# Kernel tuning notes

Hardware: AMD Instinct MI355X
Metric: run time of the kernel (lower is better)

The kernel has to match this reference:

```python
import jax, jax.numpy as jnp
import numpy as np

# Config (matches init_kwargs + Mamba2 defaults: expand=2, headdim=64, ngroups=1)
B_, C_IN, T, H, W = 4, 23, 8, 128, 128
P = 4
DM = 256
D_STATE = 16
D_CONV = 4
EXPAND = 2
D_INNER = EXPAND * DM            # 512
HEADDIM = 64
NHEADS = D_INNER // HEADDIM      # 8
CONV_DIM = D_INNER + 2 * D_STATE # 544 (ngroups=1)
D_IN_PROJ = 2 * D_INNER + 2 * D_STATE + NHEADS


def setup_inputs() -> dict:
    key = jax.random.key(0)
    ks = jax.random.split(key, 12)
    s = lambda k, shape, sc: (jax.random.normal(k, shape, jnp.float32) * sc)
    x = jax.random.normal(ks[0], (B_, C_IN, T, H, W), jnp.float32)
    patch_w = s(ks[1], (DM, C_IN, P, P), 0.05)       # Conv3d weight, depth-1 dim squeezed
    patch_b = s(ks[2], (DM,), 0.02)
    W_in = s(ks[3], (DM, D_IN_PROJ), 0.05)           # in_proj (bias=False)
    conv_w = s(ks[4], (CONV_DIM, D_CONV), 0.2)       # depthwise conv1d weight
    conv_b = s(ks[5], (CONV_DIM,), 0.02)
    dt_bias = jnp.log(jnp.expm1(jnp.exp(jax.random.uniform(ks[6], (NHEADS,), jnp.float32, jnp.log(1e-3), jnp.log(1e-1)))))
    A_log = jnp.log(jnp.arange(1, NHEADS + 1, dtype=jnp.float32))
    D_param = jnp.ones((NHEADS,), jnp.float32)
    norm_w = jnp.ones((D_INNER,), jnp.float32)
    W_out = s(ks[7], (D_INNER, DM), 0.05)            # out_proj (bias=False)
    unembed_w = s(ks[8], (DM, C_IN, P, P), 0.05)     # ConvTranspose3d weight (in,out,1,p,p)
    unembed_b = s(ks[9], (C_IN,), 0.02)
    return {"x": x, "patch_w": patch_w, "patch_b": patch_b, "W_in": W_in,
            "conv_w": conv_w, "conv_b": conv_b, "dt_bias": dt_bias, "A_log": A_log,
            "D_param": D_param, "norm_w": norm_w, "W_out": W_out,
            "unembed_w": unembed_w, "unembed_b": unembed_b}


def reference(x, patch_w, patch_b, W_in, conv_w, conv_b, dt_bias, A_log,
              D_param, norm_w, W_out, unembed_w, unembed_b):
    B, C, Tt, Hh, Ww = x.shape
    p = patch_w.shape[-1]
    Hp, Wp = Hh // p, Ww // p
    L = Tt * Hp * Wp
    # --- Conv3d patch embed (kernel (1,p,p), stride (1,p,p)) == non-overlapping patchify ---
    xr = x.reshape(B, C, Tt, Hp, p, Wp, p)
    emb = jnp.einsum('bcthiwj,dcij->bthwd', xr, patch_w) + patch_b  # [B,T,Hp,Wp,D]
    xs = emb.reshape(B, L, DM)
    # --- Mamba2 ---
    zxbcdt = xs @ W_in                                 # [B,L,2*d_inner+2*d_state+nheads]
    z = zxbcdt[:, :, :D_INNER]
    xBC = zxbcdt[:, :, D_INNER:D_INNER + CONV_DIM]
    dt = zxbcdt[:, :, D_INNER + CONV_DIM:]             # [B,L,nheads]
    # causal depthwise conv1d + silu
    xp = jnp.pad(xBC, ((0, 0), (D_CONV - 1, 0), (0, 0)))
    conv_out = conv_b + sum(xp[:, k:k + L, :] * conv_w[:, k] for k in range(D_CONV))
    xBC = jax.nn.silu(conv_out)
    xh = xBC[:, :, :D_INNER].reshape(B, L, NHEADS, HEADDIM)
    Bm = xBC[:, :, D_INNER:D_INNER + D_STATE]          # [B,L,N] (ngroups=1)
    Cm = xBC[:, :, D_INNER + D_STATE:]                 # [B,L,N]
    dt = jax.nn.softplus(dt + dt_bias)                 # [B,L,H]
    A = -jnp.exp(A_log)                                # [H]
    dA = jnp.exp(dt * A)                               # [B,L,H]
    xdt = xh * dt[..., None]                           # [B,L,H,P]
    # selective state-space scan: h_t = dA_t h_{t-1} + (dt_t x_t) B_t^T ; y_t = h_t C_t
    def step(h, inp):
        dA_t, xdt_t, B_t, C_t = inp
        h = dA_t[..., None, None] * h + jnp.einsum('bhp,bn->bhpn', xdt_t, B_t)
        y = jnp.einsum('bhpn,bn->bhp', h, C_t)
        return h, y
    inps = (dA.transpose(1, 0, 2), xdt.transpose(1, 0, 2, 3),
            Bm.transpose(1, 0, 2), Cm.transpose(1, 0, 2))
    h0 = jnp.zeros((B, NHEADS, HEADDIM, D_STATE), xs.dtype)
    _, ys = jax.lax.scan(step, h0, inps)               # [L,B,H,P]
    y = ys.transpose(1, 0, 2, 3) + D_param[None, None, :, None] * xh
    y = y.reshape(B, L, D_INNER)
    # gated RMSNorm (norm_before_gate=False): rmsnorm(y * silu(z)) * w
    yg = y * jax.nn.silu(z)
    y = yg * jax.lax.rsqrt(jnp.mean(yg * yg, axis=-1, keepdims=True) + 1e-5) * norm_w
    out_seq = y @ W_out                                # [B,L,DM]
    # --- ConvTranspose3d unembed (kernel (1,p,p), stride (1,p,p)) == un-patchify ---
    outp = out_seq.reshape(B, Tt, Hp, Wp, DM)
    un = jnp.einsum('bthwd,dcij->bcthiwj', outp, unembed_w)
    out = un.reshape(B, C, Tt, Hh, Ww) + unembed_b[None, :, None, None, None]
    return out + x
```

## Files before the change

kernel.cpp:

```cpp
#include <hip/hip_runtime.h>
#include <hip/hip_bf16.h>
#include <cstdint>
#include <cstddef>

#define B_N       4
#define C_INCH    23
#define T_N       8
#define W_IMG     128
#define L_SEQ     8192
#define BLROWS    32768
#define DM_       256
#define D_INNER_  512
#define CONV_DIM_ 544
#define D_PROJ    1064
#define KPATCH    368
#define QCH       64
#define NCH       128
#define RECW      56

typedef unsigned short ushort_t;
typedef unsigned int uint_t;
typedef __attribute__((ext_vector_type(8))) short short8;
typedef __attribute__((ext_vector_type(4))) float f32x4;

__device__ __forceinline__ float b2f(ushort_t u) {
    union { float f; uint_t u; } v; v.u = ((uint_t)u) << 16; return v.f;
}
__device__ __forceinline__ ushort_t f2b(float f) {
    union { float f; uint_t u; } v; v.f = f;
    uint_t r = v.u + 0x7fffu + ((v.u >> 16) & 1u);
    return (ushort_t)(r >> 16);
}

__device__ __forceinline__ void gload_lds16(const ushort_t* g, ushort_t* l) {
    __builtin_amdgcn_global_load_lds(
        (const __attribute__((address_space(1))) unsigned int*)g,
        (__attribute__((address_space(3))) unsigned int*)l, 16, 0, 0);
}

__device__ __forceinline__ short8 frag8(const float* q, bool live) {
    short8 f;
    if (live) {
        float4 lo = *(const float4*)q, hi = *(const float4*)(q + 4);
        f[0] = (short)f2b(lo.x); f[1] = (short)f2b(lo.y);
        f[2] = (short)f2b(lo.z); f[3] = (short)f2b(lo.w);
        f[4] = (short)f2b(hi.x); f[5] = (short)f2b(hi.y);
        f[6] = (short)f2b(hi.z); f[7] = (short)f2b(hi.w);
    } else {
        #pragma unroll
        for (int e = 0; e < 8; ++e) f[e] = 0;
    }
    return f;
}

__global__ void k_transcast(const float* __restrict__ src, ushort_t* __restrict__ dst,
                            int K, int N, const float* __restrict__ rscale) {
    int n = blockIdx.x;
    for (int k = threadIdx.x; k < K; k += 256) {
        float v = 0.f;
        if (n < N) {
            v = src[(size_t)k * N + n];
            if (rscale) v *= rscale[k];
        }
        dst[(size_t)n * K + k] = f2b(v);
    }
}

__global__ void k_castpad(const float* __restrict__ src, ushort_t* __restrict__ dst) {
    int d = blockIdx.x; int k = threadIdx.x;
    dst[d * 384 + k] = (k < KPATCH) ? f2b(src[d * KPATCH + k]) : (ushort_t)0;
}

__global__ void __launch_bounds__(256) k_pgemm(const float* __restrict__ x,
                                               const ushort_t* __restrict__ Wt,
                                               ushort_t* __restrict__ Cv,
                                               const float* __restrict__ bias) {
    __shared__ ushort_t Al[128 * 64];
    __shared__ ushort_t Bl[128 * 64];
    const int tid = threadIdx.x;
    const int w = tid >> 6, lane = tid & 63;
    const int wr = w >> 1, wc = w & 1;
    const int rowbase = blockIdx.y * 128;
    const int colbase = blockIdx.x * 128;
    const int g = lane >> 4, r = lane & 15;
    const int b  = rowbase >> 13;
    const int t  = (rowbase >> 10) & 7;
    const int hp0 = (rowbase >> 5) & 31;

    f32x4 acc[4][4];
    #pragma unroll
    for (int i = 0; i < 4; ++i)
        #pragma unroll
        for (int j = 0; j < 4; ++j) acc[i][j] = (f32x4){0.f, 0.f, 0.f, 0.f};

    for (int it = 0; it < 6; ++it) {
        int k0 = it * 64;
        __syncthreads();
        #pragma unroll
        for (int i2 = 0; i2 < 4; ++i2) {
            int s = i2 * 256 + (w << 6) + lane;
            int row = s >> 3;
            int c16 = (s & 7) ^ (row & 7);
            gload_lds16(Wt + (size_t)(colbase + row) * 384 + k0 + c16 * 8,
                        &Bl[(size_t)(i2 * 256 + (w << 6)) * 8]);
        }
        #pragma unroll
        for (int i2 = 0; i2 < 8; ++i2) {
            int idx = i2 * 256 + tid;
            int row = idx >> 4, kq = idx & 15;
            int c = (k0 >> 4) + (kq >> 2);
            int i = kq & 3;
            uint_t u0 = 0, u1 = 0;
            if (c < C_INCH) {
                int hp = hp0 + (row >> 5), wp = row & 31;
                const float4 v = *(const float4*)&x[(((size_t)(b * C_INCH + c) * T_N + t) << 14)
                                                    + (size_t)(hp * 4 + i) * W_IMG + wp * 4];
                u0 = (uint_t)f2b(v.x) | ((uint_t)f2b(v.y) << 16);
                u1 = (uint_t)f2b(v.z) | ((uint_t)f2b(v.w) << 16);
            }
            int slot = (row << 3) + ((kq >> 1) ^ (row & 7));
            *(uint2*)&Al[(size_t)slot * 8 + (kq & 1) * 4] = make_uint2(u0, u1);
        }
        __syncthreads();

        short8 af[2][4], bf[2][4];
        #pragma unroll
        for (int ks = 0; ks < 2; ++ks)
            #pragma unroll
            for (int mi = 0; mi < 4; ++mi) {
                int row = (wr << 6) + (mi << 4) + r;
                int c16 = ((ks << 2) | g) ^ (row & 7);
                af[ks][mi] = *(const short8*)&Al[(size_t)((row << 3) + c16) * 8];
            }
        #pragma unroll
        for (int ks = 0; ks < 2; ++ks)
            #pragma unroll
            for (int ni = 0; ni < 4; ++ni) {
                int row = (wc << 6) + (ni << 4) + r;
                int c16 = ((ks << 2) | g) ^ (row & 7);
                bf[ks][ni] = *(const short8*)&Bl[(size_t)((row << 3) + c16) * 8];
            }
        #pragma unroll
        for (int ks = 0; ks < 2; ++ks)
            #pragma unroll
            for (int mi = 0; mi < 4; ++mi)
                #pragma unroll
                for (int ni = 0; ni < 4; ++ni)
                    acc[mi][ni] = __builtin_amdgcn_mfma_f32_16x16x32_bf16(
                        af[ks][mi], bf[ks][ni], acc[mi][ni], 0, 0, 0);
    }

    #pragma unroll
    for (int mi = 0; mi < 4; ++mi) {
        int rw = rowbase + (wr << 6) + (mi << 4) + (g << 2);
        #pragma unroll
        for (int ni = 0; ni < 4; ++ni) {
            int col = colbase + (wc << 6) + (ni << 4) + r;
            float bv = bias[col];
            f32x4 v = acc[mi][ni];
            #pragma unroll
            for (int j = 0; j < 4; ++j)
                Cv[(size_t)(rw + j) * DM_ + col] = f2b(v[j] + bv);
        }
    }
}

template <int K, int N, bool CBF, bool ASCALE>
__global__ void __launch_bounds__(256) k_mgemm(const ushort_t* __restrict__ A, const int lda,
                                               const ushort_t* __restrict__ Wt,
                                               void* __restrict__ Cv, const int ldc, const int coff,
                                               const float* __restrict__ bias) {
    __shared__ ushort_t Al[128 * 64];
    __shared__ ushort_t Bl[128 * 64];
    const int tid = threadIdx.x;
    const int w = tid >> 6, lane = tid & 63;
    const int wr = w >> 1, wc = w & 1;
    const int rowbase = blockIdx.y * 128;
    const int colbase = blockIdx.x * 128;
    const int g = lane >> 4, r = lane & 15;

    f32x4 acc[4][4];
    #pragma unroll
    for (int i = 0; i < 4; ++i)
        #pragma unroll
        for (int j = 0; j < 4; ++j) acc[i][j] = (f32x4){0.f, 0.f, 0.f, 0.f};
    float rs[4] = {0.f, 0.f, 0.f, 0.f};

    for (int k0 = 0; k0 < K; k0 += 64) {
        __syncthreads();
        #pragma unroll
        for (int it = 0; it < 4; ++it) {
            int s = it * 256 + (w << 6) + lane;
            int row = s >> 3;
            int c16 = (s & 7) ^ (row & 7);
            gload_lds16(A + (size_t)(rowbase + row) * lda + k0 + c16 * 8,
                        &Al[(size_t)(it * 256 + (w << 6)) * 8]);
        }
        #pragma unroll
        for (int it = 0; it < 4; ++it) {
            int s = it * 256 + (w << 6) + lane;
            int row = s >> 3;
            int c16 = (s & 7) ^ (row & 7);
            gload_lds16(Wt + (size_t)(colbase + row) * K + k0 + c16 * 8,
                        &Bl[(size_t)(it * 256 + (w << 6)) * 8]);
        }
        __syncthreads();

        short8 af[2][4], bf[2][4];
        #pragma unroll
        for (int ks = 0; ks < 2; ++ks)
            #pragma unroll
            for (int mi = 0; mi < 4; ++mi) {
                int row = (wr << 6) + (mi << 4) + r;
                int c16 = ((ks << 2) | g) ^ (row & 7);
                af[ks][mi] = *(const short8*)&Al[(size_t)((row << 3) + c16) * 8];
            }
        #pragma unroll
        for (int ks = 0; ks < 2; ++ks)
            #pragma unroll
            for (int ni = 0; ni < 4; ++ni) {
                int row = (wc << 6) + (ni << 4) + r;
                int c16 = ((ks << 2) | g) ^ (row & 7);
                bf[ks][ni] = *(const short8*)&Bl[(size_t)((row << 3) + c16) * 8];
            }
        if (ASCALE) {
            #pragma unroll
            for (int ks = 0; ks < 2; ++ks)
                #pragma unroll
                for (int mi = 0; mi < 4; ++mi)
                    #pragma unroll
                    for (int e = 0; e < 8; ++e) {
                        float v = b2f((ushort_t)af[ks][mi][e]);
                        rs[mi] += v * v;
                    }
        }
        #pragma unroll
        for (int ks = 0; ks < 2; ++ks)
            #pragma unroll
            for (int mi = 0; mi < 4; ++mi)
                #pragma unroll
                for (int ni = 0; ni < 4; ++ni)
                    acc[mi][ni] = __builtin_amdgcn_mfma_f32_16x16x32_bf16(
                        af[ks][mi], bf[ks][ni], acc[mi][ni], 0, 0, 0);
    }

    #pragma unroll
    for (int mi = 0; mi < 4; ++mi) {
        int rw = rowbase + (wr << 6) + (mi << 4) + (g << 2);
        float sj[4] = {1.f, 1.f, 1.f, 1.f};
        if (ASCALE) {
            float s = rs[mi];
            s += __shfl_xor(s, 16);
            s += __shfl_xor(s, 32);
            float sc = rsqrtf(s * (1.f / 512.f) + 1e-5f);
            #pragma unroll
            for (int j = 0; j < 4; ++j) sj[j] = __shfl(sc, 4 * g + j);
        }
        #pragma unroll
        for (int ni = 0; ni < 4; ++ni) {
            int col = colbase + (wc << 6) + (ni << 4) + r;
            if (col < N) {
                float bv = bias ? bias[col] : 0.f;
                f32x4 v = acc[mi][ni];
                #pragma unroll
                for (int j = 0; j < 4; ++j) {
                    size_t cidx = (size_t)(rw + j) * ldc + coff + col;
                    float vr = v[j] * sj[j] + bv;
                    if (CBF) ((ushort_t*)Cv)[cidx] = f2b(vr);
                    else     ((float*)Cv)[cidx]   = vr;
                }
            }
        }
    }
}

__global__ void __launch_bounds__(256) k_conv(const ushort_t* __restrict__ xbcdt,
                                              const float* __restrict__ cw,
                                              const float* __restrict__ cb,
                                              const float* __restrict__ dtb,
                                              const float* __restrict__ alog,
                                              ushort_t* __restrict__ xbc,
                                              float* __restrict__ brec) {
    int tid = threadIdx.x;
    int rb = blockIdx.x * 8;
    int srb = rb & (L_SEQ - 1);
    #pragma unroll
    for (int it = 0; it < 3; ++it) {
        int ch = it * 256 + tid;
        if (ch >= 552) break;
        if (ch < CONV_DIM_) {
            float w0 = cw[ch * 4 + 0], w1 = cw[ch * 4 + 1];
            float w2 = cw[ch * 4 + 2], w3 = cw[ch * 4 + 3];
            float bias = cb[ch];
            float win[11];
            #pragma unroll
            for (int j = 0; j < 11; ++j) {
                int sj = srb + j - 3;
                win[j] = (sj >= 0) ? b2f(xbcdt[(size_t)(rb + j - 3) * 640 + ch]) : 0.f;
            }
            #pragma unroll
            for (int r = 0; r < 8; ++r) {
                float acc = bias + win[r] * w0 + win[r + 1] * w1 + win[r + 2] * w2 + win[r + 3] * w3;
                float s = acc / (1.f + __expf(-acc));
                size_t row = rb + r;
                if (ch < 512) xbc[row * 512 + ch] = f2b(s);
                else          brec[row * RECW + (ch - 512)] = s;
            }
        } else {
            int h = ch - CONV_DIM_;
            float A = -__expf(alog[h]);
            float db = dtb[h];
            #pragma unroll
            for (int r = 0; r < 8; ++r) {
                size_t row = rb + r;
                float v = b2f(xbcdt[row * 640 + ch]) + db;
                float sp = (v > 20.f) ? v : log1pf(__expf(v));
                brec[row * RECW + 32 + h] = __expf(sp * A);
                brec[row * RECW + 40 + h] = sp;
                brec[row * RECW + 48 + h] = sp * A;
            }
        }
    }
}

__global__ void __launch_bounds__(64) k_scan1m(const ushort_t* __restrict__ xbc,
                                               const float* __restrict__ brec,
                                               float* __restrict__ sbuf,
                                               float* __restrict__ cdf) {
    __shared__ ushort_t XhT[64 * 72];
    __shared__ float    Bst[64 * 20];
    __shared__ ushort_t BwT[16 * 72];
    const int c = blockIdx.x, h = blockIdx.y, b = blockIdx.z;
    const int lane = threadIdx.x;
    const int g = lane >> 4, r = lane & 15;
    const size_t row0 = (size_t)b * L_SEQ + (size_t)c * QCH;

    uint4 xw[8];
    {
        const uint4* xsrc = (const uint4*)(xbc + (row0 + lane) * 512 + h * 64);
        #pragma unroll
        for (int q = 0; q < 8; ++q) xw[q] = xsrc[q];
    }
    #pragma unroll
    for (int it2 = 0; it2 < 4; ++it2) {
        int idx = it2 * 64 + lane;
        int row = idx >> 2, q = idx & 3;
        float4 v = *(const float4*)(brec + (row0 + row) * RECW + q * 4);
        *(float4*)&Bst[row * 20 + q * 4] = v;
    }
    float ldA = brec[(row0 + lane) * RECW + 48 + h];
    float dtv = brec[(row0 + lane) * RECW + 40 + h];

    float S = ldA;
    #pragma unroll
    for (int d = 1; d < 64; d <<= 1) {
        float o = __shfl(S, (lane >= d) ? (lane - d) : 0);
        if (lane >= d) S += o;
    }
    float Stot = __shfl(S, 63);
    float wj = dtv * __expf(Stot - S);

    #pragma unroll
    for (int p = 0; p < 64; ++p) {
        uint4 v = xw[p >> 3];
        int sub = (p >> 1) & 3;
        uint_t word = (sub == 0) ? v.x : (sub == 1) ? v.y : (sub == 2) ? v.z : v.w;
        XhT[p * 72 + lane] = (ushort_t)((p & 1) ? (word >> 16) : (word & 0xffffu));
    }
    __syncthreads();

    {
        const float* bp = &Bst[lane * 20];
        float4 b0 = *(const float4*)bp;
        float4 b1 = *(const float4*)(bp + 4);
        float4 b2 = *(const float4*)(bp + 8);
        float4 b3 = *(const float4*)(bp + 12);
        float bv[16] = {b0.x,b0.y,b0.z,b0.w, b1.x,b1.y,b1.z,b1.w,
                        b2.x,b2.y,b2.z,b2.w, b3.x,b3.y,b3.z,b3.w};
        #pragma unroll
        for (int n = 0; n < 16; ++n)
            BwT[n * 72 + lane] = f2b(bv[n] * wj);
    }
    __syncthreads();

    short8 bwtf[2];
    bwtf[0] = *(const short8*)&BwT[r * 72 + 0  + g * 8];
    bwtf[1] = *(const short8*)&BwT[r * 72 + 32 + g * 8];

    size_t base = ((size_t)(b * 8 + h) * NCH + c) * 1024;
    #pragma unroll
    for (int p0t = 0; p0t < 4; ++p0t) {
        short8 a0 = *(const short8*)&XhT[(p0t * 16 + r) * 72 + 0  + g * 8];
        short8 a1 = *(const short8*)&XhT[(p0t * 16 + r) * 72 + 32 + g * 8];
        f32x4 acc = (f32x4){0.f, 0.f, 0.f, 0.f};
        acc = __builtin_amdgcn_mfma_f32_16x16x32_bf16(a0, bwtf[0], acc, 0, 0, 0);
        acc = __builtin_amdgcn_mfma_f32_16x16x32_bf16(a1, bwtf[1], acc, 0, 0, 0);
        #pragma unroll
        for (int reg = 0; reg < 4; ++reg)
            sbuf[base + (size_t)(p0t * 16 + g * 4 + reg) * 16 + r] = acc[reg];
    }
    if (lane == 63) cdf[(b * 8 + h) * NCH + c] = __expf(S);
}

__global__ void __launch_bounds__(256) k_chain(const float* __restrict__ sbuf,
                                               const float* __restrict__ cdf,
                                               float* __restrict__ hin) {
    int h = blockIdx.x, b = blockIdx.y;
    int tid = threadIdx.x;
    float4 H = make_float4(0.f, 0.f, 0.f, 0.f);
    size_t base = (size_t)((b * 8 + h) * NCH) * 1024;
    for (int c = 0; c < NCH; ++c) {
        *(float4*)&hin[base + (size_t)c * 1024 + tid * 4] = H;
        float cdfv = cdf[(b * 8 + h) * NCH + c];
        float4 S = *(const float4*)&sbuf[base + (size_t)c * 1024 + tid * 4];
        H.x = cdfv * H.x + S.x;
        H.y = cdfv * H.y + S.y;
        H.z = cdfv * H.z + S.z;
        H.w = cdfv * H.w + S.w;
    }
}

__global__ void __launch_bounds__(64) k_ssc2(const ushort_t* __restrict__ xbc,
                                             const ushort_t* __restrict__ z_bf,
                                             const float* __restrict__ brec,
                                             const float* __restrict__ Dp,
                                             const float* __restrict__ hin,
                                             ushort_t* __restrict__ yg_out) {
    __shared__ ushort_t XhT[64 * 72];
    __shared__ ushort_t Pl [64 * 72];
    __shared__ float Sl[64], Tl[64], El[64];
    const int c = blockIdx.x, h = blockIdx.y, b = blockIdx.z;
    const int lane = threadIdx.x;
    const int g = lane >> 4, r = lane & 15;
    const size_t row0 = (size_t)b * L_SEQ + (size_t)c * QCH;
    const size_t bhc = (size_t)(b * 8 + h) * NCH + c;

    uint4 xw[8];
    {
        const uint4* xsrc = (const uint4*)(xbc + (row0 + lane) * 512 + h * 64);
        #pragma unroll
        for (int q = 0; q < 8; ++q) xw[q] = xsrc[q];
    }
    #pragma unroll
    for (int it2 = 0; it2 < 8; ++it2) {
        int idx = it2 * 64 + lane;
        int row = idx >> 3, q = idx & 7;
        float4 v = *(const float4*)(brec + (row0 + row) * RECW + q * 4);
        uint_t u0 = (uint_t)f2b(v.x) | ((uint_t)f2b(v.y) << 16);
        uint_t u1 = (uint_t)f2b(v.z) | ((uint_t)f2b(v.w) << 16);
        *(uint2*)&Pl[row * 40 + q * 4] = make_uint2(u0, u1);
    }
    float ldA = brec[(row0 + lane) * RECW + 48 + h];
    float dtv = brec[(row0 + lane) * RECW + 40 + h];

    float S = ldA;
    #pragma unroll
    for (int d = 1; d < 64; d <<= 1) {
        float o = __shfl(S, (lane >= d) ? (lane - d) : 0);
        if (lane >= d) S += o;
    }
    Sl[lane] = S;
    Tl[lane] = S - __logf(dtv);
    El[lane] = __expf(S);

    #pragma unroll
    for (int p = 0; p < 64; ++p) {
        uint4 v = xw[p >> 3];
        int sub = (p >> 1) & 3;
        uint_t word = (sub == 0) ? v.x : (sub == 1) ? v.y : (sub == 2) ? v.z : v.w;
        XhT[p * 72 + lane] = (ushort_t)((p & 1) ? (word >> 16) : (word & 0xffffu));
    }
    __syncthreads();

    short8 cwf[4], bwf[4];
    #pragma unroll
    for (int t4 = 0; t4 < 4; ++t4) {
        if (g < 2) {
            bwf[t4] = *(const short8*)&Pl[(t4 * 16 + r) * 40 + 0  + g * 8];
            cwf[t4] = *(const short8*)&Pl[(t4 * 16 + r) * 40 + 16 + g * 8];
        } else {
            #pragma unroll
            for (int e = 0; e < 8; ++e) { bwf[t4][e] = 0; cwf[t4][e] = 0; }
        }
    }
    __syncthreads();

    #pragma unroll
    for (int j0t = 0; j0t < 4; ++j0t) {
        #pragma unroll
        for (int i0t = 0; i0t < 4; ++i0t) {
            f32x4 m = (f32x4){0.f, 0.f, 0.f, 0.f};
            m = __builtin_amdgcn_mfma_f32_16x16x32_bf16(bwf[j0t], cwf[i0t], m, 0, 0, 0);
            int i = i0t * 16 + r;
            float si = Sl[i];
            float4 tj = *(const float4*)&Tl[j0t * 16 + g * 4];
            ushort_t pv[4];
            #pragma unroll
            for (int reg = 0; reg < 4; ++reg) {
                int j = j0t * 16 + g * 4 + reg;
                float tjv = (reg == 0) ? tj.x : (reg == 1) ? tj.y : (reg == 2) ? tj.z : tj.w;
                float mask = (j <= i) ? __expf(si - tjv) : 0.f;
                pv[reg] = f2b(m[reg] * mask);
            }
            uint2 packed = make_uint2((uint_t)pv[0] | ((uint_t)pv[1] << 16),
                                      (uint_t)pv[2] | ((uint_t)pv[3] << 16));
            *(uint2*)&Pl[i * 72 + j0t * 16 + g * 4] = packed;
        }
    }
    __syncthreads();

    short8 xhf[4][2];
    #pragma unroll
    for (int p0t = 0; p0t < 4; ++p0t)
        #pragma unroll
        for (int kk = 0; kk < 2; ++kk)
            xhf[p0t][kk] = *(const short8*)&XhT[(p0t * 16 + r) * 72 + kk * 32 + g * 8];
    short8 hinf[4];
    #pragma unroll
    for (int p0t = 0; p0t < 4; ++p0t)
        hinf[p0t] = frag8(hin + bhc * 1024 + (size_t)(p0t * 16 + r) * 16 + g * 8, g < 2);

    const float Dh = Dp[h];

    #pragma unroll
    for (int i0t = 0; i0t < 4; ++i0t) {
        short8 pa0 = *(const short8*)&Pl[(i0t * 16 + r) * 72 + 0  + g * 8];
        short8 pa1 = *(const short8*)&Pl[(i0t * 16 + r) * 72 + 32 + g * 8];
        float4 e4 = *(const float4*)&El[i0t * 16 + g * 4];
        #pragma unroll
        for (int p0t = 0; p0t < 4; ++p0t) {
            f32x4 acc = (f32x4){0.f, 0.f, 0.f, 0.f};
            acc = __builtin_amdgcn_mfma_f32_16x16x32_bf16(cwf[i0t], hinf[p0t], acc, 0, 0, 0);
            acc[0] *= e4.x; acc[1] *= e4.y; acc[2] *= e4.z; acc[3] *= e4.w;
            acc = __builtin_amdgcn_mfma_f32_16x16x32_bf16(pa0, xhf[p0t][0], acc, 0, 0, 0);
            acc = __builtin_amdgcn_mfma_f32_16x16x32_bf16(pa1, xhf[p0t][1], acc, 0, 0, 0);
            int p = p0t * 16 + r;
            #pragma unroll
            for (int reg = 0; reg < 4; ++reg) {
                int i = i0t * 16 + g * 4 + reg;
                size_t row = row0 + i;
                float xhv = b2f(XhT[p * 72 + i]);
                float y = acc[reg] + Dh * xhv;
                float zz = b2f(z_bf[row * 512 + h * 64 + p]);
                float ygv = y * (zz / (1.f + __expf(-zz)));
                yg_out[row * 512 + h * 64 + p] = f2b(ygv);
            }
        }
    }
}

__global__ void __launch_bounds__(256) k_scatter(const ushort_t* __restrict__ tmp,
                                                 const float* __restrict__ ub,
                                                 const float* __restrict__ xin,
                                                 float* __restrict__ out) {
    int tid = threadIdx.x;
    int w = tid & 127;
    int h = (blockIdx.x << 1) | (tid >> 7);
    int c = blockIdx.y >> 3, t = blockIdx.y & 7;
    int b = blockIdx.z;
    size_t row = (size_t)b * L_SEQ + t * 1024 + (h >> 2) * 32 + (w >> 2);
    int kk = c * 16 + (h & 3) * 4 + (w & 3);
    size_t oidx = (((size_t)(b * C_INCH + c) * T_N + t) << 14) + (size_t)h * W_IMG + w;
    out[oidx] = b2f(tmp[row * KPATCH + kk]) + ub[c] + xin[oidx];
}

extern "C" void kernel_launch(void* const* d_in, const int* in_sizes, int n_in,
                              void* d_out, int out_size, void* d_ws, size_t ws_size,
                              hipStream_t stream) {
    const float* x       = (const float*)d_in[0];
    const float* patch_w = (const float*)d_in[1];
    const float* patch_b = (const float*)d_in[2];
    const float* W_in    = (const float*)d_in[3];
    const float* conv_w  = (const float*)d_in[4];
    const float* conv_b  = (const float*)d_in[5];
    const float* dt_bias = (const float*)d_in[6];
    const float* A_log   = (const float*)d_in[7];
    const float* D_param = (const float*)d_in[8];
    const float* norm_w  = (const float*)d_in[9];
    const float* W_out   = (const float*)d_in[10];
    const float* unemb_w = (const float*)d_in[11];
    const float* unemb_b = (const float*)d_in[12];
    float* out = (float*)d_out;

    char* p = (char*)d_ws;
    ushort_t* scratch = (ushort_t*)p; p += (size_t)BLROWS * 384 * 2;
    float* cdf  = (float*)p;   p += (size_t)32 * NCH * 4;
    float* sbuf = (float*)p;   p += (size_t)32 * NCH * 1024 * 4;
    float* hin  = (float*)p;   p += (size_t)32 * NCH * 1024 * 4;
    float* brec = (float*)p;   p += (size_t)BLROWS * RECW * 4;
    ushort_t* Wt_p   = (ushort_t*)p; p += (size_t)256 * 384 * 2;
    ushort_t* Wt_in  = (ushort_t*)p; p += (size_t)1152 * 256 * 2;
    ushort_t* Wt_out = (ushort_t*)p; p += (size_t)256 * 512 * 2;
    ushort_t* Wt_un  = (ushort_t*)p; p += (size_t)384 * 256 * 2;
    ushort_t* xs     = (ushort_t*)p; p += (size_t)BLROWS * DM_ * 2;
    ushort_t* xbc    = (ushort_t*)p; p += (size_t)BLROWS * 512 * 2;
    ushort_t* z_bf   = (ushort_t*)p; p += (size_t)BLROWS * 512 * 2;
    ushort_t* xbcdt  = (ushort_t*)p; p += (size_t)BLROWS * 640 * 2;
    size_t need = (size_t)(p - (char*)d_ws);
    if (ws_size < need) return;

    ushort_t* tmp = scratch;
    ushort_t* yg  = xbcdt;

    k_castpad<<<256, 384, 0, stream>>>(patch_w, Wt_p);
    k_transcast<<<1152, 256, 0, stream>>>(W_in, Wt_in, 256, 1064, nullptr);
    k_transcast<<<256, 256, 0, stream>>>(W_out, Wt_out, 512, 256, norm_w);
    k_transcast<<<384, 256, 0, stream>>>(unemb_w, Wt_un, 256, 368, nullptr);

    k_pgemm<<<dim3(2, 256), 256, 0, stream>>>(x, Wt_p, xs, patch_b);

    k_mgemm<256, 512, true, false><<<dim3(4, 256), 256, 0, stream>>>(xs, 256, Wt_in, z_bf, 512, 0, nullptr);
    k_mgemm<256, 552, true, false><<<dim3(5, 256), 256, 0, stream>>>(xs, 256, Wt_in + (size_t)512 * 256, xbcdt, 640, 0, nullptr);

    k_conv<<<BLROWS / 8, 256, 0, stream>>>(xbcdt, conv_w, conv_b, dt_bias, A_log, xbc, brec);

    k_scan1m<<<dim3(NCH, 8, 4), 64, 0, stream>>>(xbc, brec, sbuf, cdf);
    k_chain<<<dim3(8, 4), 256, 0, stream>>>(sbuf, cdf, hin);
    k_ssc2<<<dim3(NCH, 8, 4), 64, 0, stream>>>(xbc, z_bf, brec, D_param, hin, yg);

    k_mgemm<512, 256, true, true><<<dim3(2, 256), 256, 0, stream>>>(yg, 512, Wt_out, xs, DM_, 0, nullptr);

    k_mgemm<256, 368, true, false><<<dim3(3, 256), 256, 0, stream>>>(xs, 256, Wt_un, tmp, KPATCH, 0, nullptr);

    k_scatter<<<dim3(64, 184, 4), 256, 0, stream>>>(tmp, unemb_b, x, out);
}
```

Measured before the change: 250.3 us.

## Split scan chunk kernels across four waves per block

k_scan1m and k_ssc2 now launch with 256 threads (four wavefronts) instead of one wavefront per chunk. The XhT transpose staging and the brec loads are spread over all waves, and each wave handles one 16-row tile of the MFMA loops that a single wave used to run serially. The cumulative-sum prefix and the cdf write stay on wave 0, so the kernels need extra barriers, including a raw s_barrier placed inside divergent branches. The aim is more parallelism per chunk and shorter per-wave serial work, at the cost of more synchronisation and a larger block footprint.

After: 253.9 us. Within noise of the previous version (+1.4%).

```diff
diff --git a/kernel.cpp b/kernel.cpp
--- a/kernel.cpp
+++ b/kernel.cpp
@@ -323,53 +323,54 @@
     }
 }
 
-__global__ void __launch_bounds__(64) k_scan1m(const ushort_t* __restrict__ xbc,
-                                               const float* __restrict__ brec,
-                                               float* __restrict__ sbuf,
-                                               float* __restrict__ cdf) {
+__device__ __forceinline__ void stage_xht(const ushort_t* __restrict__ xbc,
+                                          size_t row0, int h, int tid,
+                                          ushort_t* __restrict__ XhT) {
+    int j = tid & 63, q4 = tid >> 6;
+    const uint4* xsrc = (const uint4*)(xbc + (row0 + j) * 512 + h * 64);
+    uint4 xa = xsrc[q4 * 2], xb = xsrc[q4 * 2 + 1];
+    #pragma unroll
+    for (int pp = 0; pp < 16; ++pp) {
+        int p = q4 * 16 + pp;
+        uint4 v = (pp < 8) ? xa : xb;
+        int sub = (pp >> 1) & 3;
+        uint_t word = (sub == 0) ? v.x : (sub == 1) ? v.y : (sub == 2) ? v.z : v.w;
+        XhT[p * 72 + j] = (ushort_t)((pp & 1) ? (word >> 16) : (word & 0xffffu));
+    }
+}
+
+__global__ void __launch_bounds__(256) k_scan1m(const ushort_t* __restrict__ xbc,
+                                                const float* __restrict__ brec,
+                                                float* __restrict__ sbuf,
+                                                float* __restrict__ cdf) {
     __shared__ ushort_t XhT[64 * 72];
     __shared__ float    Bst[64 * 20];
     __shared__ ushort_t BwT[16 * 72];
     const int c = blockIdx.x, h = blockIdx.y, b = blockIdx.z;
-    const int lane = threadIdx.x;
+    const int tid = threadIdx.x;
+    const int w = tid >> 6, lane = tid & 63;
     const int g = lane >> 4, r = lane & 15;
     const size_t row0 = (size_t)b * L_SEQ + (size_t)c * QCH;
 
-    uint4 xw[8];
     {
-        const uint4* xsrc = (const uint4*)(xbc + (row0 + lane) * 512 + h * 64);
-        #pragma unroll
-        for (int q = 0; q < 8; ++q) xw[q] = xsrc[q];
-    }
-    #pragma unroll
-    for (int it2 = 0; it2 < 4; ++it2) {
-        int idx = it2 * 64 + lane;
-        int row = idx >> 2, q = idx & 3;
+        int row = tid >> 2, q = tid & 3;
         float4 v = *(const float4*)(brec + (row0 + row) * RECW + q * 4);
         *(float4*)&Bst[row * 20 + q * 4] = v;
     }
-    float ldA = brec[(row0 + lane) * RECW + 48 + h];
-    float dtv = brec[(row0 + lane) * RECW + 40 + h];
-
-    float S = ldA;
-    #pragma unroll
-    for (int d = 1; d < 64; d <<= 1) {
-        float o = __shfl(S, (lane >= d) ? (lane - d) : 0);
-        if (lane >= d) S += o;
-    }
-    float Stot = __shfl(S, 63);
-    float wj = dtv * __expf(Stot - S);
-
-    #pragma unroll
-    for (int p = 0; p < 64; ++p) {
-        uint4 v = xw[p >> 3];
-        int sub = (p >> 1) & 3;
-        uint_t word = (sub == 0) ? v.x : (sub == 1) ? v.y : (sub == 2) ? v.z : v.w;
-        XhT[p * 72 + lane] = (ushort_t)((p & 1) ? (word >> 16) : (word & 0xffffu));
-    }
-    __syncthreads();
-
-    {
+    stage_xht(xbc, row0, h, tid, XhT);
+
+    if (w == 0) {
+        float ldA = brec[(row0 + lane) * RECW + 48 + h];
+        float dtv = brec[(row0 + lane) * RECW + 40 + h];
+        float S = ldA;
+        #pragma unroll
+        for (int d = 1; d < 64; d <<= 1) {
+            float o = __shfl(S, (lane >= d) ? (lane - d) : 0);
+            if (lane >= d) S += o;
+        }
+        float Stot = __shfl(S, 63);
+        float wj = dtv * __expf(Stot - S);
+        __builtin_amdgcn_s_barrier();
         const float* bp = &Bst[lane * 20];
         float4 b0 = *(const float4*)bp;
         float4 b1 = *(const float4*)(bp + 4);
@@ -380,6 +381,9 @@
         #pragma unroll
         for (int n = 0; n < 16; ++n)
             BwT[n * 72 + lane] = f2b(bv[n] * wj);
+        if (lane == 63) cdf[(b * 8 + h) * NCH + c] = __expf(S);
+    } else {
+        __builtin_amdgcn_s_barrier();
     }
     __syncthreads();
 
@@ -388,8 +392,8 @@
     bwtf[1] = *(const short8*)&BwT[r * 72 + 32 + g * 8];
 
     size_t base = ((size_t)(b * 8 + h) * NCH + c) * 1024;
-    #pragma unroll
-    for (int p0t = 0; p0t < 4; ++p0t) {
+    {
+        int p0t = w;
         short8 a0 = *(const short8*)&XhT[(p0t * 16 + r) * 72 + 0  + g * 8];
         short8 a1 = *(const short8*)&XhT[(p0t * 16 + r) * 72 + 32 + g * 8];
         f32x4 acc = (f32x4){0.f, 0.f, 0.f, 0.f};
@@ -399,7 +403,6 @@
         for (int reg = 0; reg < 4; ++reg)
             sbuf[base + (size_t)(p0t * 16 + g * 4 + reg) * 16 + r] = acc[reg];
     }
-    if (lane == 63) cdf[(b * 8 + h) * NCH + c] = __expf(S);
 }
 
 __global__ void __launch_bounds__(256) k_chain(const float* __restrict__ sbuf,
@@ -420,55 +423,45 @@
     }
 }
 
-__global__ void __launch_bounds__(64) k_ssc2(const ushort_t* __restrict__ xbc,
-                                             const ushort_t* __restrict__ z_bf,
-                                             const float* __restrict__ brec,
-                                             const float* __restrict__ Dp,
-                                             const float* __restrict__ hin,
-                                             ushort_t* __restrict__ yg_out) {
+__global__ void __launch_bounds__(256) k_ssc2(const ushort_t* __restrict__ xbc,
+                                              const ushort_t* __restrict__ z_bf,
+                                              const float* __restrict__ brec,
+                                              const float* __restrict__ Dp,
+                                              const float* __restrict__ hin,
+                                              ushort_t* __restrict__ yg_out) {
     __shared__ ushort_t XhT[64 * 72];
     __shared__ ushort_t Pl [64 * 72];
     __shared__ float Sl[64], Tl[64], El[64];
     const int c = blockIdx.x, h = blockIdx.y, b = blockIdx.z;
-    const int lane = threadIdx.x;
+    const int tid = threadIdx.x;
+    const int w = tid >> 6, lane = tid & 63;
     const int g = lane >> 4, r = lane & 15;
     const size_t row0 = (size_t)b * L_SEQ + (size_t)c * QCH;
     const size_t bhc = (size_t)(b * 8 + h) * NCH + c;
 
-    uint4 xw[8];
-    {
-        const uint4* xsrc = (const uint4*)(xbc + (row0 + lane) * 512 + h * 64);
-        #pragma unroll
-        for (int q = 0; q < 8; ++q) xw[q] = xsrc[q];
-    }
-    #pragma unroll
-    for (int it2 = 0; it2 < 8; ++it2) {
-        int idx = it2 * 64 + lane;
+    #pragma unroll
+    for (int it2 = 0; it2 < 2; ++it2) {
+        int idx = it2 * 256 + tid;
         int row = idx >> 3, q = idx & 7;
         float4 v = *(const float4*)(brec + (row0 + row) * RECW + q * 4);
         uint_t u0 = (uint_t)f2b(v.x) | ((uint_t)f2b(v.y) << 16);
         uint_t u1 = (uint_t)f2b(v.z) | ((uint_t)f2b(v.w) << 16);
         *(uint2*)&Pl[row * 40 + q * 4] = make_uint2(u0, u1);
     }
-    float ldA = brec[(row0 + lane) * RECW + 48 + h];
-    float dtv = brec[(row0 + lane) * RECW + 40 + h];
-
-    float S = ldA;
-    #pragma unroll
-    for (int d = 1; d < 64; d <<= 1) {
-        float o = __shfl(S, (lane >= d) ? (lane - d) : 0);
-        if (lane >= d) S += o;
-    }
-    Sl[lane] = S;
-    Tl[lane] = S - __logf(dtv);
-    El[lane] = __expf(S);
-
-    #pragma unroll
-    for (int p = 0; p < 64; ++p) {
-        uint4 v = xw[p >> 3];
-        int sub = (p >> 1) & 3;
-        uint_t word = (sub == 0) ? v.x : (sub == 1) ? v.y : (sub == 2) ? v.z : v.w;
-        XhT[p * 72 + lane] = (ushort_t)((p & 1) ? (word >> 16) : (word & 0xffffu));
+    stage_xht(xbc, row0, h, tid, XhT);
+
+    if (w == 0) {
+        float ldA = brec[(row0 + lane) * RECW + 48 + h];
+        float dtv = brec[(row0 + lane) * RECW + 40 + h];
+        float S = ldA;
+        #pragma unroll
+        for (int d = 1; d < 64; d <<= 1) {
+            float o = __shfl(S, (lane >= d) ? (lane - d) : 0);
+            if (lane >= d) S += o;
+        }
+        Sl[lane] = S;
+        Tl[lane] = S - __logf(dtv);
+        El[lane] = __expf(S);
     }
     __syncthreads();
 
@@ -485,14 +478,14 @@
     }
     __syncthreads();
 
-    #pragma unroll
-    for (int j0t = 0; j0t < 4; ++j0t) {
-        #pragma unroll
-        for (int i0t = 0; i0t < 4; ++i0t) {
+    {
+        const int i0t = w;
+        int i = i0t * 16 + r;
+        float si = Sl[i];
+        #pragma unroll
+        for (int j0t = 0; j0t < 4; ++j0t) {
             f32x4 m = (f32x4){0.f, 0.f, 0.f, 0.f};
             m = __builtin_amdgcn_mfma_f32_16x16x32_bf16(bwf[j0t], cwf[i0t], m, 0, 0, 0);
-            int i = i0t * 16 + r;
-            float si = Sl[i];
             float4 tj = *(const float4*)&Tl[j0t * 16 + g * 4];
             ushort_t pv[4];
             #pragma unroll
@@ -522,8 +515,8 @@
 
     const float Dh = Dp[h];
 
-    #pragma unroll
-    for (int i0t = 0; i0t < 4; ++i0t) {
+    {
+        const int i0t = w;
         short8 pa0 = *(const short8*)&Pl[(i0t * 16 + r) * 72 + 0  + g * 8];
         short8 pa1 = *(const short8*)&Pl[(i0t * 16 + r) * 72 + 32 + g * 8];
         float4 e4 = *(const float4*)&El[i0t * 16 + g * 4];
@@ -614,9 +607,9 @@
 
     k_conv<<<BLROWS / 8, 256, 0, stream>>>(xbcdt, conv_w, conv_b, dt_bias, A_log, xbc, brec);
 
-    k_scan1m<<<dim3(NCH, 8, 4), 64, 0, stream>>>(xbc, brec, sbuf, cdf);
+    k_scan1m<<<dim3(NCH, 8, 4), 256, 0, stream>>>(xbc, brec, sbuf, cdf);
     k_chain<<<dim3(8, 4), 256, 0, stream>>>(sbuf, cdf, hin);
-    k_ssc2<<<dim3(NCH, 8, 4), 64, 0, stream>>>(xbc, z_bf, brec, D_param, hin, yg);
+    k_ssc2<<<dim3(NCH, 8, 4), 256, 0, stream>>>(xbc, z_bf, brec, D_param, hin, yg);
 
     k_mgemm<512, 256, true, true><<<dim3(2, 256), 256, 0, stream>>>(yg, 512, Wt_out, xs, DM_, 0, nullptr);
 
```
